# Kernel optimization log

Hardware: AMD Instinct MI355X
Metric: run time of the kernel (lower is better)

The kernel has to match this reference:

```python
import jax, jax.numpy as jnp
import numpy as np

B, T, H = 16, 64, 256  # batch, timesteps (= num stacked layers), hidden
L = T                  # MultiRNNCell([cell]*timesteps): layers == timesteps, shared weights


def setup_inputs() -> dict:
    key = jax.random.key(0)
    k1, k2, k3 = jax.random.split(key, 3)
    x = jax.random.normal(k1, (B, T, H), dtype=jnp.float32)
    init_state = jax.random.normal(k2, (L, 2, B, H), dtype=jnp.float32) * 0.1  # [L, (c,h), B, H]
    W = jax.random.normal(k3, (2 * H, 4 * H), dtype=jnp.float32) / np.sqrt(2 * H)
    b = jnp.zeros((4 * H,), dtype=jnp.float32)
    return {"x": x, "init_state": init_state, "W": W, "b": b}


def reference(x, init_state, W, b):
    # TF LSTMCell math: gates order (i, j, f, o), forget_bias = 1.0
    c0 = init_state[:, 0]  # [L,B,H]
    h0 = init_state[:, 1]  # [L,B,H]

    def layer_fn(inp, st):
        # inp: [B,H] input to this layer; st = (c,h) each [B,H]
        lc, lh = st
        z = jnp.concatenate([inp, lh], axis=-1) @ W + b  # [B,4H]
        i, j, f, o = jnp.split(z, 4, axis=-1)
        nc = jax.nn.sigmoid(f + 1.0) * lc + jax.nn.sigmoid(i) * jnp.tanh(j)
        nh = jax.nn.sigmoid(o) * jnp.tanh(nc)
        return nh, (nc, nh)  # carry = input to next layer; ys = new per-layer state

    def step(carry, xt):
        # carry: (c,h) each [L,B,H]; xt: [B,H]
        c, h = carry
        top_h, (nc, nh) = jax.lax.scan(layer_fn, xt, (c, h))
        return (nc, nh), top_h

    (_, _), ys = jax.lax.scan(step, (c0, h0), jnp.transpose(x, (1, 0, 2)))  # ys: [T,B,H]
    return jnp.transpose(ys, (1, 0, 2))  # [B,T,H] top-layer outputs (dynamic_rnn outputs)
```

## Files before the change

kernel.cpp:

```cpp
#include <hip/hip_runtime.h>

typedef _Float16 half8 __attribute__((ext_vector_type(8)));
typedef float f32x4 __attribute__((ext_vector_type(4)));

#define SCOPE __HIP_MEMORY_SCOPE_AGENT

constexpr size_t OFF_PROG = 0;
constexpr size_t OFF_H    = 65536;
constexpr size_t SLOT_STRIDE = (size_t)64 * 16 * 128;

__device__ __forceinline__ size_t Widx(int l, int b, int wi) {
  return ((size_t)l * 16 + b) * 128 + wi;
}
__device__ __forceinline__ float sigm(float v) { return 1.0f / (1.0f + __expf(-v)); }
__device__ __forceinline__ float tanh_(float v) { return 1.0f - 2.0f / (__expf(2.0f * v) + 1.0f); }

__global__ void init_ws(const float* __restrict__ init_state, char* ws) {
  int* prog = (int*)(ws + OFF_PROG);
  unsigned long long* Hw = (unsigned long long*)(ws + OFF_H);
  const int tid = blockIdx.x * 256 + threadIdx.x;
  if (tid < 256) prog[tid] = -1;
  for (int e = tid; e < 64 * 16 * 128; e += 65536) {
    const int wi = e & 127, b = (e >> 7) & 15, l = e >> 11;
    Hw[Widx(l, b, wi)] = 0xFFFE00000000ULL;
    union { _Float16 f; unsigned short s; } h0, h1;
    h0.f = (_Float16)init_state[((l * 2 + 1) * 16 + b) * 256 + 2 * wi];
    h1.f = (_Float16)init_state[((l * 2 + 1) * 16 + b) * 256 + 2 * wi + 1];
    Hw[SLOT_STRIDE + Widx(l, b, wi)] =
        (unsigned long long)h0.s | ((unsigned long long)h1.s << 16) | (0xFFFFULL << 32);
  }
}

__global__ __launch_bounds__(256, 1) void lstm_mfma(
    const float* __restrict__ x, const float* __restrict__ init_state,
    const float* __restrict__ W, const float* __restrict__ bias,
    float* __restrict__ out, char* ws) {
  int* prog = (int*)(ws + OFF_PROG);
  unsigned long long* Hw = (unsigned long long*)(ws + OFF_H);

  const int tid = threadIdx.x;
  const int wg = blockIdx.x;
  const int l = wg >> 2, r = wg & 3;
  const int wv = tid >> 6, lane = tid & 63;

  __shared__ alignas(16) _Float16 aLds[16 * 64 * 8];
  __shared__ alignas(16) float zLds[16 * 260];
  __shared__ unsigned short hLds[16 * 64];

  half8 wreg[64];
#pragma unroll
  for (int q = 0; q < 4; ++q) {
    const int nl = (wv * 4 + q) * 16 + (lane & 15);
    const int col = (nl & 3) * 256 + r * 64 + (nl >> 2);
#pragma unroll
    for (int kb = 0; kb < 16; ++kb) {
      const int k0 = kb * 32 + (lane >> 4) * 8;
      const float* src = W + (size_t)k0 * 1024 + col;
      half8 hv;
#pragma unroll
      for (int jj = 0; jj < 8; ++jj) hv[jj] = (_Float16)src[(size_t)jj * 1024];
      wreg[q * 16 + kb] = hv;
    }
  }

  const int hu = tid & 63, b4 = tid >> 6;
  const int gu = r * 64 + hu;
  float creg[4];
#pragma unroll
  for (int bb = 0; bb < 4; ++bb)
    creg[bb] = init_state[((l * 2 + 0) * 16 + (b4 * 4 + bb)) * 256 + gu];
  const float bi_ = bias[0 * 256 + gu], bj_ = bias[1 * 256 + gu];
  const float bf_ = bias[2 * 256 + gu], bo_ = bias[3 * 256 + gu];

  int kbA[4], lnA[4];
  size_t wbase[4];
#pragma unroll
  for (int i = 0; i < 4; ++i) {
    const int e = i * 256 + tid, kb = e >> 6, ln = e & 63;
    const int m = ln & 15, k0 = kb * 32 + (ln >> 4) * 8;
    kbA[i] = kb; lnA[i] = ln;
    wbase[i] = (i < 2) ? (l > 0 ? Widx(l - 1, m, k0 >> 1) : 0)
                       : Widx(l, m, (k0 - 256) >> 1);
  }

  for (int t = 0; t < 64; ++t) {
    const int slotCur = t & 1, slotPrev = (t + 1) & 1;
    const unsigned short tagIn = (unsigned short)t;
    const unsigned short tagOwn = (unsigned short)(t - 1);

    if (l == 0) {
#pragma unroll
      for (int i = 0; i < 2; ++i) {
        const int kb = kbA[i], ln = lnA[i];
        const int m = ln & 15, k0 = kb * 32 + (ln >> 4) * 8;
        const float* xs = x + ((size_t)m * 64 + t) * 256 + k0;
        half8 hv;
#pragma unroll
        for (int jj = 0; jj < 8; ++jj) hv[jj] = (_Float16)xs[jj];
        *(half8*)&aLds[(size_t)(kb * 64 + ln) * 8] = hv;
      }
    }

    unsigned pend = (l == 0) ? 0xFF00u : 0xFFFFu;
    bool bp = !(tid == 0 && l < 63 && t >= 2);
    int round = 0;
    while (pend || !bp) {
      bool fast = true;
      if (round >= 2 && l > 0 && (pend & 0x00FFu)) {
        int pl = __hip_atomic_load(&prog[(l - 1) * 4 + r], __ATOMIC_RELAXED, SCOPE);
        fast = (pl >= t);
      }
      if (fast && pend) {
        unsigned long long wv_[16];
#pragma unroll
        for (int i = 0; i < 4; ++i) {
          const unsigned long long* sp =
              Hw + ((i < 2 ? slotCur : slotPrev) ? SLOT_STRIDE : 0) + wbase[i];
#pragma unroll
          for (int j = 0; j < 4; ++j) {
            const int b_ = i * 4 + j;
            if ((pend >> b_) & 1u)
              wv_[b_] = __hip_atomic_load(sp + j, __ATOMIC_RELAXED, SCOPE);
          }
        }
#pragma unroll
        for (int i = 0; i < 4; ++i) {
          unsigned* dp = (unsigned*)&aLds[(size_t)(kbA[i] * 64 + lnA[i]) * 8];
          const unsigned short exp_ = (i < 2) ? tagIn : tagOwn;
#pragma unroll
          for (int j = 0; j < 4; ++j) {
            const int b_ = i * 4 + j;
            if ((pend >> b_) & 1u) {
              const unsigned long long wd = wv_[b_];
              if ((unsigned short)(wd >> 32) == exp_) {
                dp[j] = (unsigned)wd;
                pend &= ~(1u << b_);
              }
            }
          }
        }
      }
      if (!bp) {
        const int need = t - 2;
        int p0 = __hip_atomic_load(&prog[(l + 1) * 4 + 0], __ATOMIC_RELAXED, SCOPE);
        int p1 = __hip_atomic_load(&prog[(l + 1) * 4 + 1], __ATOMIC_RELAXED, SCOPE);
        int p2 = __hip_atomic_load(&prog[(l + 1) * 4 + 2], __ATOMIC_RELAXED, SCOPE);
        int p3 = __hip_atomic_load(&prog[(l + 1) * 4 + 3], __ATOMIC_RELAXED, SCOPE);
        bp = (p0 >= need) && (p1 >= need) && (p2 >= need) && (p3 >= need);
      }
      if (pend || !bp) {
        ++round;
        if (round > 4000000) break;
        if (fast) __builtin_amdgcn_s_sleep(1);
        else      __builtin_amdgcn_s_sleep(16);
      }
    }
    __syncthreads();
    if (tid == 0) __hip_atomic_store(&prog[wg], t, __ATOMIC_RELAXED, SCOPE);

    f32x4 acc[4] = {{0.f, 0.f, 0.f, 0.f}, {0.f, 0.f, 0.f, 0.f},
                    {0.f, 0.f, 0.f, 0.f}, {0.f, 0.f, 0.f, 0.f}};
#pragma unroll
    for (int kb = 0; kb < 16; ++kb) {
      half8 a = *(const half8*)&aLds[(kb * 64 + lane) * 8];
#pragma unroll
      for (int q = 0; q < 4; ++q)
        acc[q] = __builtin_amdgcn_mfma_f32_16x16x32_f16(a, wreg[q * 16 + kb], acc[q], 0, 0, 0);
    }

#pragma unroll
    for (int q = 0; q < 4; ++q) {
      const int nl = (wv * 4 + q) * 16 + (lane & 15);
      const int m0 = (lane >> 4) * 4;
#pragma unroll
      for (int rg = 0; rg < 4; ++rg) zLds[(m0 + rg) * 260 + nl] = acc[q][rg];
    }
    __syncthreads();

#pragma unroll
    for (int bb = 0; bb < 4; ++bb) {
      const int b = b4 * 4 + bb;
      f32x4 zg = *(const f32x4*)&zLds[b * 260 + hu * 4];
      const float iv = zg[0] + bi_, jv = zg[1] + bj_;
      const float fv = zg[2] + bf_, ov = zg[3] + bo_;
      const float nc = sigm(fv + 1.0f) * creg[bb] + sigm(iv) * tanh_(jv);
      const float nh = sigm(ov) * tanh_(nc);
      creg[bb] = nc;
      union { _Float16 f; unsigned short s; } cv;
      cv.f = (_Float16)nh;
      hLds[b * 64 + hu] = cv.s;
      if (l == 63) out[((size_t)b * 64 + t) * 256 + gu] = nh;
    }
    __syncthreads();

    {
      const int b = tid >> 4, lw0 = (tid & 15) * 2;
#pragma unroll
      for (int q = 0; q < 2; ++q) {
        const int lw = lw0 + q, u0 = 2 * lw;
        unsigned lo = (unsigned)hLds[b * 64 + u0] | ((unsigned)hLds[b * 64 + u0 + 1] << 16);
        unsigned long long wd =
            (unsigned long long)lo | ((unsigned long long)tagIn << 32);
        __hip_atomic_store(Hw + (slotCur ? SLOT_STRIDE : 0) + Widx(l, b, r * 32 + lw),
                           wd, __ATOMIC_RELAXED, SCOPE);
      }
    }
  }
}

extern "C" void kernel_launch(void* const* d_in, const int* in_sizes, int n_in,
                              void* d_out, int out_size, void* d_ws,
                              size_t ws_size, hipStream_t stream) {
  const float* x          = (const float*)d_in[0];
  const float* init_state = (const float*)d_in[1];
  const float* W          = (const float*)d_in[2];
  const float* bias       = (const float*)d_in[3];
  float* out = (float*)d_out;
  char* ws   = (char*)d_ws;

  init_ws<<<256, 256, 0, stream>>>(init_state, ws);
  lstm_mfma<<<256, 256, 0, stream>>>(x, init_state, W, bias, out, ws);
}
```

Measured before the change: 813.2 us.

## Remap workgroups to co-locate adjacent layers and use workgroup-scope polling loads

Remaps blockIdx to (layer, rank) so that neighbouring layers land on the same XCD (round-robin dispatch assumption), aiming to keep the producer/consumer handoff within one L2. Polling loads alternate between workgroup scope (cheaper, may hit caches) and agent scope to escape stale values. Sleep is removed on the fast path, and a damping check on predecessor progress is delayed. The risk is that workgroup-scope loads may read stale cached data, which would lengthen polling. The correctness of the dispatch-to-XCD mapping is also assumed rather than guaranteed.

```diff
diff --git a/kernel.cpp b/kernel.cpp
--- a/kernel.cpp
+++ b/kernel.cpp
@@ -3,7 +3,8 @@
 typedef _Float16 half8 __attribute__((ext_vector_type(8)));
 typedef float f32x4 __attribute__((ext_vector_type(4)));
 
-#define SCOPE __HIP_MEMORY_SCOPE_AGENT
+#define SC_AGENT __HIP_MEMORY_SCOPE_AGENT
+#define SC_WG    __HIP_MEMORY_SCOPE_WORKGROUP
 
 constexpr size_t OFF_PROG = 0;
 constexpr size_t OFF_H    = 65536;
@@ -11,6 +12,9 @@
 
 __device__ __forceinline__ size_t Widx(int l, int b, int wi) {
   return ((size_t)l * 16 + b) * 128 + wi;
+}
+__device__ __forceinline__ int wgid(int l, int r) {
+  return (((l & 7) * 4 + r) << 3) | (l >> 3);
 }
 __device__ __forceinline__ float sigm(float v) { return 1.0f / (1.0f + __expf(-v)); }
 __device__ __forceinline__ float tanh_(float v) { return 1.0f - 2.0f / (__expf(2.0f * v) + 1.0f); }
@@ -40,7 +44,8 @@
 
   const int tid = threadIdx.x;
   const int wg = blockIdx.x;
-  const int l = wg >> 2, r = wg & 3;
+  const int l = ((wg & 7) << 3) | (wg >> 5);
+  const int r = (wg >> 3) & 3;
   const int wv = tid >> 6, lane = tid & 63;
 
   __shared__ alignas(16) _Float16 aLds[16 * 64 * 8];
@@ -83,6 +88,12 @@
                        : Widx(l, m, (k0 - 256) >> 1);
   }
 
+  int* const progIn = &prog[wgid(l > 0 ? l - 1 : 0, r)];
+  int* const bpp0 = &prog[wgid(l < 63 ? l + 1 : 63, 0)];
+  int* const bpp1 = &prog[wgid(l < 63 ? l + 1 : 63, 1)];
+  int* const bpp2 = &prog[wgid(l < 63 ? l + 1 : 63, 2)];
+  int* const bpp3 = &prog[wgid(l < 63 ? l + 1 : 63, 3)];
+
   for (int t = 0; t < 64; ++t) {
     const int slotCur = t & 1, slotPrev = (t + 1) & 1;
     const unsigned short tagIn = (unsigned short)t;
@@ -105,12 +116,15 @@
     bool bp = !(tid == 0 && l < 63 && t >= 2);
     int round = 0;
     while (pend || !bp) {
-      bool fast = true;
-      if (round >= 2 && l > 0 && (pend & 0x00FFu)) {
-        int pl = __hip_atomic_load(&prog[(l - 1) * 4 + r], __ATOMIC_RELAXED, SCOPE);
-        fast = (pl >= t);
-      }
-      if (fast && pend) {
+      const bool esc = (round & 1) != 0;
+      bool damp = false;
+      if (round >= 8 && l > 0 && (pend & 0x00FFu)) {
+        int pl = ((round & 7) == 1)
+                     ? __hip_atomic_load(progIn, __ATOMIC_RELAXED, SC_AGENT)
+                     : __hip_atomic_load(progIn, __ATOMIC_RELAXED, SC_WG);
+        damp = (pl < t);
+      }
+      if (pend && !damp) {
         unsigned long long wv_[16];
 #pragma unroll
         for (int i = 0; i < 4; ++i) {
@@ -120,7 +134,8 @@
           for (int j = 0; j < 4; ++j) {
             const int b_ = i * 4 + j;
             if ((pend >> b_) & 1u)
-              wv_[b_] = __hip_atomic_load(sp + j, __ATOMIC_RELAXED, SCOPE);
+              wv_[b_] = esc ? __hip_atomic_load(sp + j, __ATOMIC_RELAXED, SC_AGENT)
+                            : __hip_atomic_load(sp + j, __ATOMIC_RELAXED, SC_WG);
           }
         }
 #pragma unroll
@@ -142,21 +157,28 @@
       }
       if (!bp) {
         const int need = t - 2;
-        int p0 = __hip_atomic_load(&prog[(l + 1) * 4 + 0], __ATOMIC_RELAXED, SCOPE);
-        int p1 = __hip_atomic_load(&prog[(l + 1) * 4 + 1], __ATOMIC_RELAXED, SCOPE);
-        int p2 = __hip_atomic_load(&prog[(l + 1) * 4 + 2], __ATOMIC_RELAXED, SCOPE);
-        int p3 = __hip_atomic_load(&prog[(l + 1) * 4 + 3], __ATOMIC_RELAXED, SCOPE);
+        int p0, p1, p2, p3;
+        if (esc) {
+          p0 = __hip_atomic_load(bpp0, __ATOMIC_RELAXED, SC_AGENT);
+          p1 = __hip_atomic_load(bpp1, __ATOMIC_RELAXED, SC_AGENT);
+          p2 = __hip_atomic_load(bpp2, __ATOMIC_RELAXED, SC_AGENT);
+          p3 = __hip_atomic_load(bpp3, __ATOMIC_RELAXED, SC_AGENT);
+        } else {
+          p0 = __hip_atomic_load(bpp0, __ATOMIC_RELAXED, SC_WG);
+          p1 = __hip_atomic_load(bpp1, __ATOMIC_RELAXED, SC_WG);
+          p2 = __hip_atomic_load(bpp2, __ATOMIC_RELAXED, SC_WG);
+          p3 = __hip_atomic_load(bpp3, __ATOMIC_RELAXED, SC_WG);
+        }
         bp = (p0 >= need) && (p1 >= need) && (p2 >= need) && (p3 >= need);
       }
       if (pend || !bp) {
         ++round;
-        if (round > 4000000) break;
-        if (fast) __builtin_amdgcn_s_sleep(1);
-        else      __builtin_amdgcn_s_sleep(16);
+        if (round > 2000000) break;
+        if (damp) __builtin_amdgcn_s_sleep(4);
       }
     }
     __syncthreads();
-    if (tid == 0) __hip_atomic_store(&prog[wg], t, __ATOMIC_RELAXED, SCOPE);
+    if (tid == 0) __hip_atomic_store(&prog[wg], t, __ATOMIC_RELAXED, SC_AGENT);
 
     f32x4 acc[4] = {{0.f, 0.f, 0.f, 0.f}, {0.f, 0.f, 0.f, 0.f},
                     {0.f, 0.f, 0.f, 0.f}, {0.f, 0.f, 0.f, 0.f}};
@@ -202,7 +224,7 @@
         unsigned long long wd =
             (unsigned long long)lo | ((unsigned long long)tagIn << 32);
         __hip_atomic_store(Hw + (slotCur ? SLOT_STRIDE : 0) + Widx(l, b, r * 32 + lw),
-                           wd, __ATOMIC_RELAXED, SCOPE);
+                           wd, __ATOMIC_RELAXED, SC_AGENT);
       }
     }
   }
```

Measured after the change: 797.1 us. -2.0%, faster.

## Restructure inter-workgroup polling with cache-bypassing loads and separate backpressure wait

Applied to the files above, without the earlier changes.

The single combined spin loop is split into three phases. First, a coarse wait on the upstream layer's progress counter. Second, a dedicated backpressure wait in which thread 0 reads all four downstream counters with one dwordx4 load. Third, a tight tag-polling loop that uses inline-asm global loads with sc0 sc1 cache bits and sleeps only occasionally. The goal is to shorten the latency between a producer publishing h and the consumer seeing it, and to stop backpressure checks from slowing the data polling. The tighter spinning adds memory traffic, and the loop iteration caps are lower.

```diff
diff --git a/kernel.cpp b/kernel.cpp
--- a/kernel.cpp
+++ b/kernel.cpp
@@ -2,8 +2,9 @@
 
 typedef _Float16 half8 __attribute__((ext_vector_type(8)));
 typedef float f32x4 __attribute__((ext_vector_type(4)));
-
-#define SCOPE __HIP_MEMORY_SCOPE_AGENT
+typedef unsigned int u32x4 __attribute__((ext_vector_type(4)));
+
+#define SC_AGENT __HIP_MEMORY_SCOPE_AGENT
 
 constexpr size_t OFF_PROG = 0;
 constexpr size_t OFF_H    = 65536;
@@ -14,6 +15,10 @@
 }
 __device__ __forceinline__ float sigm(float v) { return 1.0f / (1.0f + __expf(-v)); }
 __device__ __forceinline__ float tanh_(float v) { return 1.0f - 2.0f / (__expf(2.0f * v) + 1.0f); }
+
+#define POLL_LD(dst, base, OFS)                                              \
+  asm volatile("global_load_dwordx2 %0, %1, off offset:" #OFS " sc0 sc1"     \
+               : "=v"(dst) : "v"(base))
 
 __global__ void init_ws(const float* __restrict__ init_state, char* ws) {
   int* prog = (int*)(ws + OFF_PROG);
@@ -83,10 +88,13 @@
                        : Widx(l, m, (k0 - 256) >> 1);
   }
 
+  int* const progIn = (l > 0) ? &prog[(l - 1) * 4 + r] : prog;
+  int* const bpBase = (l < 63) ? &prog[(l + 1) * 4] : prog;
+
   for (int t = 0; t < 64; ++t) {
     const int slotCur = t & 1, slotPrev = (t + 1) & 1;
-    const unsigned short tagIn = (unsigned short)t;
-    const unsigned short tagOwn = (unsigned short)(t - 1);
+    const unsigned expIn = (unsigned)(unsigned short)t;
+    const unsigned expOwn = (unsigned)(unsigned short)(t - 1);
 
     if (l == 0) {
 #pragma unroll
@@ -101,62 +109,80 @@
       }
     }
 
+    if (l > 0) {
+      int pl = __hip_atomic_load(progIn, __ATOMIC_RELAXED, SC_AGENT);
+      int g = 0;
+      while (pl < t - 1) {
+        __builtin_amdgcn_s_sleep(8);
+        pl = __hip_atomic_load(progIn, __ATOMIC_RELAXED, SC_AGENT);
+        if (++g > 400000) break;
+      }
+    }
+
+    if (tid == 0 && l < 63 && t >= 2) {
+      const int need = t - 2;
+      int g = 0;
+      while (true) {
+        u32x4 pv;
+        asm volatile("global_load_dwordx4 %0, %1, off sc0 sc1" : "=v"(pv) : "v"(bpBase));
+        asm volatile("s_waitcnt vmcnt(0)" ::: "memory");
+        __builtin_amdgcn_sched_barrier(0);
+        if ((int)pv[0] >= need && (int)pv[1] >= need &&
+            (int)pv[2] >= need && (int)pv[3] >= need) break;
+        __builtin_amdgcn_s_sleep(2);
+        if (++g > 400000) break;
+      }
+    }
+
     unsigned pend = (l == 0) ? 0xFF00u : 0xFFFFu;
-    bool bp = !(tid == 0 && l < 63 && t >= 2);
     int round = 0;
-    while (pend || !bp) {
-      bool fast = true;
-      if (round >= 2 && l > 0 && (pend & 0x00FFu)) {
-        int pl = __hip_atomic_load(&prog[(l - 1) * 4 + r], __ATOMIC_RELAXED, SCOPE);
-        fast = (pl >= t);
-      }
-      if (fast && pend) {
-        unsigned long long wv_[16];
-#pragma unroll
-        for (int i = 0; i < 4; ++i) {
-          const unsigned long long* sp =
-              Hw + ((i < 2 ? slotCur : slotPrev) ? SLOT_STRIDE : 0) + wbase[i];
-#pragma unroll
-          for (int j = 0; j < 4; ++j) {
-            const int b_ = i * 4 + j;
-            if ((pend >> b_) & 1u)
-              wv_[b_] = __hip_atomic_load(sp + j, __ATOMIC_RELAXED, SCOPE);
-          }
-        }
-#pragma unroll
-        for (int i = 0; i < 4; ++i) {
-          unsigned* dp = (unsigned*)&aLds[(size_t)(kbA[i] * 64 + lnA[i]) * 8];
-          const unsigned short exp_ = (i < 2) ? tagIn : tagOwn;
-#pragma unroll
-          for (int j = 0; j < 4; ++j) {
-            const int b_ = i * 4 + j;
-            if ((pend >> b_) & 1u) {
-              const unsigned long long wd = wv_[b_];
-              if ((unsigned short)(wd >> 32) == exp_) {
-                dp[j] = (unsigned)wd;
-                pend &= ~(1u << b_);
-              }
+    while (pend) {
+      unsigned long long wv_[16];
+      const unsigned long long* sp0 = Hw + (slotCur ? SLOT_STRIDE : 0) + wbase[0];
+      const unsigned long long* sp1 = Hw + (slotCur ? SLOT_STRIDE : 0) + wbase[1];
+      const unsigned long long* sp2 = Hw + (slotPrev ? SLOT_STRIDE : 0) + wbase[2];
+      const unsigned long long* sp3 = Hw + (slotPrev ? SLOT_STRIDE : 0) + wbase[3];
+      if (pend & 0x0001u) POLL_LD(wv_[0],  sp0, 0);
+      if (pend & 0x0002u) POLL_LD(wv_[1],  sp0, 8);
+      if (pend & 0x0004u) POLL_LD(wv_[2],  sp0, 16);
+      if (pend & 0x0008u) POLL_LD(wv_[3],  sp0, 24);
+      if (pend & 0x0010u) POLL_LD(wv_[4],  sp1, 0);
+      if (pend & 0x0020u) POLL_LD(wv_[5],  sp1, 8);
+      if (pend & 0x0040u) POLL_LD(wv_[6],  sp1, 16);
+      if (pend & 0x0080u) POLL_LD(wv_[7],  sp1, 24);
+      if (pend & 0x0100u) POLL_LD(wv_[8],  sp2, 0);
+      if (pend & 0x0200u) POLL_LD(wv_[9],  sp2, 8);
+      if (pend & 0x0400u) POLL_LD(wv_[10], sp2, 16);
+      if (pend & 0x0800u) POLL_LD(wv_[11], sp2, 24);
+      if (pend & 0x1000u) POLL_LD(wv_[12], sp3, 0);
+      if (pend & 0x2000u) POLL_LD(wv_[13], sp3, 8);
+      if (pend & 0x4000u) POLL_LD(wv_[14], sp3, 16);
+      if (pend & 0x8000u) POLL_LD(wv_[15], sp3, 24);
+      asm volatile("s_waitcnt vmcnt(0)" ::: "memory");
+      __builtin_amdgcn_sched_barrier(0);
+#pragma unroll
+      for (int i = 0; i < 4; ++i) {
+        unsigned* dp = (unsigned*)&aLds[(size_t)(kbA[i] * 64 + lnA[i]) * 8];
+        const unsigned exp_ = (i < 2) ? expIn : expOwn;
+#pragma unroll
+        for (int j = 0; j < 4; ++j) {
+          const int b_ = i * 4 + j;
+          if ((pend >> b_) & 1u) {
+            const unsigned long long wd = wv_[b_];
+            if ((unsigned)(wd >> 32) == exp_) {
+              dp[j] = (unsigned)wd;
+              pend &= ~(1u << b_);
             }
           }
         }
       }
-      if (!bp) {
-        const int need = t - 2;
-        int p0 = __hip_atomic_load(&prog[(l + 1) * 4 + 0], __ATOMIC_RELAXED, SCOPE);
-        int p1 = __hip_atomic_load(&prog[(l + 1) * 4 + 1], __ATOMIC_RELAXED, SCOPE);
-        int p2 = __hip_atomic_load(&prog[(l + 1) * 4 + 2], __ATOMIC_RELAXED, SCOPE);
-        int p3 = __hip_atomic_load(&prog[(l + 1) * 4 + 3], __ATOMIC_RELAXED, SCOPE);
-        bp = (p0 >= need) && (p1 >= need) && (p2 >= need) && (p3 >= need);
-      }
-      if (pend || !bp) {
-        ++round;
-        if (round > 4000000) break;
-        if (fast) __builtin_amdgcn_s_sleep(1);
-        else      __builtin_amdgcn_s_sleep(16);
+      if (pend) {
+        if (++round > 500000) break;
+        if ((round & 15) == 0) __builtin_amdgcn_s_sleep(1);
       }
     }
     __syncthreads();
-    if (tid == 0) __hip_atomic_store(&prog[wg], t, __ATOMIC_RELAXED, SCOPE);
+    if (tid == 0) __hip_atomic_store(&prog[l * 4 + r], t, __ATOMIC_RELAXED, SC_AGENT);
 
     f32x4 acc[4] = {{0.f, 0.f, 0.f, 0.f}, {0.f, 0.f, 0.f, 0.f},
                     {0.f, 0.f, 0.f, 0.f}, {0.f, 0.f, 0.f, 0.f}};
@@ -200,9 +226,9 @@
         const int lw = lw0 + q, u0 = 2 * lw;
         unsigned lo = (unsigned)hLds[b * 64 + u0] | ((unsigned)hLds[b * 64 + u0 + 1] << 16);
         unsigned long long wd =
-            (unsigned long long)lo | ((unsigned long long)tagIn << 32);
+            (unsigned long long)lo | ((unsigned long long)expIn << 32);
         __hip_atomic_store(Hw + (slotCur ? SLOT_STRIDE : 0) + Widx(l, b, r * 32 + lw),
-                           wd, __ATOMIC_RELAXED, SCOPE);
+                           wd, __ATOMIC_RELAXED, SC_AGENT);
       }
     }
   }
```

Result: faster. 767.5 us (-5.6%).
